# Optimization experiments

Measured on AMD Instinct MI355X. Metric: run time of the kernel, lower is better.

The kernel has to match this reference:

```python
import jax, jax.numpy as jnp
import numpy as np

B, N, DIM, H, K = 2, 8192, 256, 8, 32
HD = DIM // H


def setup_inputs() -> dict:
    key = jax.random.key(0)
    ks = jax.random.split(key, 10)
    s = 1.0 / np.sqrt(DIM)
    return {
        "x": jax.random.normal(ks[0], (B, N, DIM), jnp.float32),
        "xyz": jax.random.normal(ks[1], (B, N, 3), jnp.float32),
        "idx": jax.random.randint(ks[2], (B, N, K), 0, N, jnp.int32),
        "Wq": jax.random.normal(ks[3], (DIM, DIM), jnp.float32) * s,
        "bq": jnp.zeros((DIM,), jnp.float32),
        "Wk": jax.random.normal(ks[4], (DIM, DIM), jnp.float32) * s,
        "bk": jnp.zeros((DIM,), jnp.float32),
        "Wv": jax.random.normal(ks[5], (DIM, DIM), jnp.float32) * s,
        "bv": jnp.zeros((DIM,), jnp.float32),
        "Wo": jax.random.normal(ks[6], (DIM, DIM), jnp.float32) * s,
        "bo": jnp.zeros((DIM,), jnp.float32),
        "W1": jax.random.normal(ks[7], (3, 32), jnp.float32) * 0.5,
        "b1": jnp.zeros((32,), jnp.float32),
        "W2": jax.random.normal(ks[8], (32, H), jnp.float32) * 0.2,
        "b2": jnp.zeros((H,), jnp.float32),
    }


def reference(x, xyz, idx, Wq, bq, Wk, bk, Wv, bv, Wo, bo, W1, b1, W2, b2):
    Bn, Nn, C = x.shape
    k = idx.shape[-1]
    q = (x @ Wq + bq).reshape(Bn, Nn, H, HD)          # [B,N,H,hd]
    kf = (x @ Wk + bk).reshape(Bn, Nn, H, HD)
    vf = (x @ Wv + bv).reshape(Bn, Nn, H, HD)
    # gather k neighbors per point (per-batch fancy indexing)
    gather = jax.vmap(lambda f, i: f[i])               # [N,H,hd],[N,k] -> [N,k,H,hd]
    kn = gather(kf, idx)                               # [B,N,k,H,hd]
    vn = gather(vf, idx)
    nxyz = jax.vmap(lambda p, i: p[i])(xyz, idx)       # [B,N,k,3]
    rel = xyz[:, :, None, :] - nxyz                    # [B,N,k,3]
    bias = jax.nn.relu(rel @ W1 + b1) @ W2 + b2        # [B,N,k,H]
    scores = jnp.einsum('bnhd,bnkhd->bnhk', q, kn) / np.sqrt(HD).astype(np.float32)
    scores = scores + bias.transpose(0, 1, 3, 2)       # [B,N,H,k]
    attn = jax.nn.softmax(scores, axis=-1)
    out = jnp.einsum('bnhk,bnkhd->bnhd', attn, vn).reshape(Bn, Nn, C)
    return out @ Wo + bo
```

## Files before the change

### kernel.cpp

```cpp
#include <hip/hip_runtime.h>
#include <hip/hip_bf16.h>

typedef unsigned int uint32;
typedef unsigned short ushort;
typedef __attribute__((ext_vector_type(4))) float floatx4;
typedef __attribute__((ext_vector_type(8))) __bf16 bf16x8;

#define NPTS 8192
#define HSZ 524288

__device__ __forceinline__ ushort f2bf(float f) {
    uint32 u = __float_as_uint(f);
    uint32 r = (u + 0x7fffu + ((u >> 16) & 1u)) >> 16;
    return (ushort)r;
}
__device__ __forceinline__ float bf1(ushort u) { return __uint_as_float((uint32)u << 16); }
__device__ __forceinline__ float bflo(uint32 u) { return __uint_as_float(u << 16); }
__device__ __forceinline__ float bfhi(uint32 u) { return __uint_as_float(u & 0xffff0000u); }

__global__ __launch_bounds__(256) void prep_kernel(
    const float* __restrict__ x, const float* __restrict__ xyz, const int* __restrict__ idx,
    const float* __restrict__ Wq, const float* __restrict__ Wk,
    const float* __restrict__ Wv, const float* __restrict__ Wo,
    const float* __restrict__ bq, const float* __restrict__ bk, const float* __restrict__ bv,
    const float* __restrict__ W1, const float* __restrict__ b1,
    const float* __restrict__ W2, const float* __restrict__ b2,
    ushort* __restrict__ xb, ushort* __restrict__ Wqkvt, ushort* __restrict__ Wot,
    float* __restrict__ biasqkv, ushort* __restrict__ bias_hg) {
    const int bi = blockIdx.x;
    const int tid = threadIdx.x;
    if (bi < 4096) {
        int i = (bi * 256 + tid) * 4;
        float4 v = *(const float4*)(x + i);
        ushort4 o;
        o.x = f2bf(v.x); o.y = f2bf(v.y); o.z = f2bf(v.z); o.w = f2bf(v.w);
        *(ushort4*)(xb + i) = o;
    } else if (bi < 5120) {
        int f = (bi - 4096) * 256 + tid;
        if (f < 768 * 256) {
            int n = f >> 8, k = f & 255;
            int seg = n >> 8, nc = n & 255;
            const float* W = (seg == 0) ? Wq : (seg == 1) ? Wk : Wv;
            Wqkvt[f] = f2bf(W[k * 256 + nc]);
        } else {
            int g = f - 768 * 256;
            int n = g >> 8, k = g & 255;
            Wot[g] = f2bf(Wo[k * 256 + n]);
        }
        if (f < 768) biasqkv[f] = (f < 256) ? bq[f] : (f < 512) ? bk[f - 256] : bv[f - 512];
    } else {
        __shared__ float W1s[96], b1s[32], W2s[256], b2s[8];
        if (tid < 96) W1s[tid] = W1[tid];
        if (tid < 32) b1s[tid] = b1[tid];
        W2s[tid] = W2[tid];
        if (tid < 8) b2s[tid] = b2[tid];
        __syncthreads();
        const int wid = tid >> 6, lane = tid & 63;
        const int s = lane >> 5, j = lane & 31;
        const int p = (bi - 5120) * 8 + wid * 2 + s;
        const int b = p >> 13, n = p & 8191;
        const int nj = idx[(size_t)p * 32 + j];
        const size_t pb = ((size_t)b * NPTS + n) * 3;
        const size_t nb = ((size_t)b * NPTS + nj) * 3;
        const float rx = xyz[pb + 0] - xyz[nb + 0];
        const float ry = xyz[pb + 1] - xyz[nb + 1];
        const float rz = xyz[pb + 2] - xyz[nb + 2];
        float acc[8];
#pragma unroll
        for (int h = 0; h < 8; ++h) acc[h] = b2s[h];
#pragma unroll
        for (int u = 0; u < 32; ++u) {
            float hv = rx * W1s[u] + ry * W1s[32 + u] + rz * W1s[64 + u] + b1s[u];
            hv = fmaxf(hv, 0.f);
#pragma unroll
            for (int h = 0; h < 8; ++h) acc[h] += hv * W2s[u * 8 + h];
        }
#pragma unroll
        for (int h = 0; h < 8; ++h) bias_hg[(size_t)h * HSZ + p * 32 + j] = f2bf(acc[h]);
    }
}

__global__ __launch_bounds__(256) void gemm_qkv(const ushort* __restrict__ A,
                                                const ushort* __restrict__ Wt,
                                                const float* __restrict__ bias,
                                                ushort* __restrict__ qh, ushort* __restrict__ kh,
                                                ushort* __restrict__ vh) {
    __shared__ __align__(16) ushort As[128 * 64];
    __shared__ __align__(16) ushort Bs[128 * 64];
    const int tid = threadIdx.x;
    const int w = tid >> 6, lane = tid & 63;
    const int m0 = blockIdx.y * 128, n0 = blockIdx.x * 128;
    const int wm = (w & 1) * 64, wn = (w >> 1) * 64;

    floatx4 acc[4][4] = {};

    for (int kt = 0; kt < 256; kt += 64) {
        __syncthreads();
#pragma unroll
        for (int c4 = 0; c4 < 4; ++c4) {
            const int c = w * 4 + c4;
            const int r = c * 8 + (lane >> 3);
            const int gseg = (lane & 7) ^ (r & 7);
            const char* ga = (const char*)(A + (size_t)(m0 + r) * 256 + kt) + gseg * 16;
            const char* gb = (const char*)(Wt + (size_t)(n0 + r) * 256 + kt) + gseg * 16;
            __builtin_amdgcn_global_load_lds((const __attribute__((address_space(1))) void*)ga,
                                             (__attribute__((address_space(3))) void*)((char*)As + c * 1024),
                                             16, 0, 0);
            __builtin_amdgcn_global_load_lds((const __attribute__((address_space(1))) void*)gb,
                                             (__attribute__((address_space(3))) void*)((char*)Bs + c * 1024),
                                             16, 0, 0);
        }
        __syncthreads();

        bf16x8 af[2][4], bg[2][4];
#pragma unroll
        for (int kk = 0; kk < 2; ++kk) {
            const int s = kk * 4 + (lane >> 4);
            const int phys = s ^ (lane & 7);
#pragma unroll
            for (int i = 0; i < 4; ++i) {
                af[kk][i] = *(const bf16x8*)((const char*)As + (wm + i * 16 + (lane & 15)) * 128 + phys * 16);
                bg[kk][i] = *(const bf16x8*)((const char*)Bs + (wn + i * 16 + (lane & 15)) * 128 + phys * 16);
            }
        }
#pragma unroll
        for (int kk = 0; kk < 2; ++kk)
#pragma unroll
            for (int mi = 0; mi < 4; ++mi)
#pragma unroll
                for (int ni = 0; ni < 4; ++ni)
                    acc[mi][ni] = __builtin_amdgcn_mfma_f32_16x16x32_bf16(af[kk][mi], bg[kk][ni], acc[mi][ni], 0, 0, 0);
    }

#pragma unroll
    for (int ni = 0; ni < 4; ++ni) {
        const int col = n0 + wn + ni * 16 + (lane & 15);
        const int seg = col >> 8;
        const int head = (col >> 5) & 7;
        const int dim = col & 31;
        ushort* segp = (seg == 0) ? qh : (seg == 1) ? kh : vh;
        const float bv = bias[col];
#pragma unroll
        for (int mi = 0; mi < 4; ++mi) {
            const int row0 = m0 + wm + mi * 16 + (lane >> 4) * 4;
#pragma unroll
            for (int r = 0; r < 4; ++r)
                segp[(size_t)head * HSZ + (size_t)(row0 + r) * 32 + dim] = f2bf(acc[mi][ni][r] + bv);
        }
    }
}

__global__ __launch_bounds__(256) void gemm_mfma64(const ushort* __restrict__ A,
                                                   const ushort* __restrict__ Wt,
                                                   const float* __restrict__ bias,
                                                   float* __restrict__ outv, int N) {
    __shared__ __align__(16) ushort As[64 * 32];
    __shared__ __align__(16) ushort Bs[64 * 32];
    const int tid = threadIdx.x;
    const int w = tid >> 6, lane = tid & 63;
    const int m0 = blockIdx.y * 64, n0 = blockIdx.x * 64;
    const int row = tid >> 2;
    const int col16 = (tid & 3) * 16;

    floatx4 acc[4] = {};

    for (int kt = 0; kt < 256; kt += 32) {
        __syncthreads();
        {
            const char* ga = (const char*)(A + (size_t)(m0 + row) * 256 + kt) + col16;
            const char* gb = (const char*)(Wt + (size_t)(n0 + row) * 256 + kt) + col16;
            __builtin_amdgcn_global_load_lds((const __attribute__((address_space(1))) void*)ga,
                                             (__attribute__((address_space(3))) void*)((char*)As + w * 1024),
                                             16, 0, 0);
            __builtin_amdgcn_global_load_lds((const __attribute__((address_space(1))) void*)gb,
                                             (__attribute__((address_space(3))) void*)((char*)Bs + w * 1024),
                                             16, 0, 0);
        }
        __syncthreads();

        bf16x8 af = *(const bf16x8*)&As[(w * 16 + (lane & 15)) * 32 + (lane >> 4) * 8];
        bf16x8 bg[4];
#pragma unroll
        for (int ni = 0; ni < 4; ++ni)
            bg[ni] = *(const bf16x8*)&Bs[(ni * 16 + (lane & 15)) * 32 + (lane >> 4) * 8];
#pragma unroll
        for (int ni = 0; ni < 4; ++ni)
            acc[ni] = __builtin_amdgcn_mfma_f32_16x16x32_bf16(af, bg[ni], acc[ni], 0, 0, 0);
    }

#pragma unroll
    for (int ni = 0; ni < 4; ++ni) {
        const int col = n0 + ni * 16 + (lane & 15);
        const float bv = bias[col];
        const int row0 = m0 + w * 16 + (lane >> 4) * 4;
#pragma unroll
        for (int r = 0; r < 4; ++r)
            outv[(size_t)(row0 + r) * N + col] = acc[ni][r] + bv;
    }
}

__global__ __launch_bounds__(256) void attn_kernel(
    const ushort* __restrict__ qh, const ushort* __restrict__ kh, const ushort* __restrict__ vh,
    const int* __restrict__ idx, const ushort* __restrict__ bias_hg, ushort* __restrict__ out) {
    __shared__ __align__(16) float q_s[4][2][32];
    __shared__ float e_s[4][2][32];
    __shared__ uint32 off_s[4][2][32];
    __shared__ float ssum_s[4][2];

    const int tid = threadIdx.x, wid = tid >> 6, lane = tid & 63;
    const int h = blockIdx.x >> 11;
    const int pg = blockIdx.x & 2047;
    const int pbase = pg * 8 + wid * 2;

    const char* kh_h = (const char*)(kh + (size_t)h * HSZ);
    const char* vh_h = (const char*)(vh + (size_t)h * HSZ);

    const int s = lane >> 5, j = lane & 31;
    const int p = pbase + s;
    const int b = p >> 13;

    off_s[wid][s][j] = (uint32)(idx[(size_t)p * 32 + j] + b * NPTS) * 64u;
    q_s[wid][s][j] = bf1(qh[(size_t)h * HSZ + p * 32 + j]);
    __syncthreads();

    {
        const uint4* kp = (const uint4*)(kh_h + off_s[wid][s][j]);
        float d = 0.f;
#pragma unroll
        for (int c = 0; c < 4; ++c) {
            uint4 kv = kp[c];
            float4 qa = *(const float4*)&q_s[wid][s][c * 8];
            float4 qb = *(const float4*)&q_s[wid][s][c * 8 + 4];
            d += bflo(kv.x) * qa.x + bfhi(kv.x) * qa.y
               + bflo(kv.y) * qa.z + bfhi(kv.y) * qa.w
               + bflo(kv.z) * qb.x + bfhi(kv.z) * qb.y
               + bflo(kv.w) * qb.z + bfhi(kv.w) * qb.w;
        }
        const float sc = d * 0.17677669529663687f + bf1(bias_hg[(size_t)h * HSZ + p * 32 + j]);
        const float e = __expf(sc);
        float ssum = e;
#pragma unroll
        for (int msk = 16; msk >= 1; msk >>= 1) ssum += __shfl_xor(ssum, msk, 64);
        e_s[wid][s][j] = e;
        if (j == 0) ssum_s[wid][s] = ssum;
    }
    __syncthreads();

    {
        const int s2 = lane >> 5, hj = (lane >> 4) & 1, d2 = lane & 15;
        const int p2 = pbase + s2;
        const float rinv = __builtin_amdgcn_rcpf(ssum_s[wid][s2]);
        float ax = 0.f, ay = 0.f;
#pragma unroll
        for (int jj = 0; jj < 16; ++jj) {
            const int j2 = hj * 16 + jj;
            const float wgt = e_s[wid][s2][j2];
            const uint32 v = *(const uint32*)(vh_h + off_s[wid][s2][j2] + d2 * 4);
            ax += wgt * bflo(v);
            ay += wgt * bfhi(v);
        }
        ax += __shfl_xor(ax, 16, 64);
        ay += __shfl_xor(ay, 16, 64);
        if (hj == 0) {
            const uint32 o = (uint32)f2bf(ax * rinv) | ((uint32)f2bf(ay * rinv) << 16);
            *(uint32*)(out + (size_t)p2 * 256 + h * 32 + d2 * 2) = o;
        }
    }
}

extern "C" void kernel_launch(void* const* d_in, const int* in_sizes, int n_in,
                              void* d_out, int out_size, void* d_ws, size_t ws_size,
                              hipStream_t stream) {
    const float* x   = (const float*)d_in[0];
    const float* xyz = (const float*)d_in[1];
    const int*   idx = (const int*)d_in[2];
    const float* Wq = (const float*)d_in[3];
    const float* bq = (const float*)d_in[4];
    const float* Wk = (const float*)d_in[5];
    const float* bk = (const float*)d_in[6];
    const float* Wv = (const float*)d_in[7];
    const float* bv = (const float*)d_in[8];
    const float* Wo = (const float*)d_in[9];
    const float* bo = (const float*)d_in[10];
    const float* W1 = (const float*)d_in[11];
    const float* b1 = (const float*)d_in[12];
    const float* W2 = (const float*)d_in[13];
    const float* b2 = (const float*)d_in[14];

    char* wsb = (char*)d_ws;
    ushort* x_bf    = (ushort*)wsb;
    ushort* aout_bf = x_bf;
    ushort* qh      = (ushort*)(wsb + 8388608);
    ushort* kh      = (ushort*)(wsb + 16777216);
    ushort* vh      = (ushort*)(wsb + 25165824);
    ushort* bias_hg = (ushort*)(wsb + 33554432);
    ushort* Wqkvt   = (ushort*)(wsb + 41943040);
    ushort* Wot     = (ushort*)(wsb + 42336256);
    float*  biasqkv = (float*)(wsb + 42467328);

    prep_kernel<<<7168, 256, 0, stream>>>(x, xyz, idx, Wq, Wk, Wv, Wo, bq, bk, bv,
                                          W1, b1, W2, b2, x_bf, Wqkvt, Wot, biasqkv, bias_hg);

    gemm_qkv<<<dim3(6, 128), 256, 0, stream>>>(x_bf, Wqkvt, biasqkv, qh, kh, vh);

    attn_kernel<<<16384, 256, 0, stream>>>(qh, kh, vh, idx, bias_hg, aout_bf);

    gemm_mfma64<<<dim3(4, 256), 256, 0, stream>>>(aout_bf, Wot, bo, (float*)d_out, 256);
}
```

Before: 184.4 us.

## Prefetch V gathers before score compute and precompute neighbor offsets in prep

The attention kernel now issues all V-row gathers right after the first barrier, so they overlap with the K dot products and softmax instead of waiting on them. Neighbor byte offsets are precomputed in the prep kernel and read directly, and the scalar bias is loaded early. The block size drops from 256 to 128 threads with double the grid and a launch bound of 6 blocks per CU. This spends 16 extra registers per thread on prefetched values and adds an offsets buffer written by prep.

```diff
diff --git a/kernel.cpp b/kernel.cpp
--- a/kernel.cpp
+++ b/kernel.cpp
@@ -26,7 +26,7 @@
     const float* __restrict__ W1, const float* __restrict__ b1,
     const float* __restrict__ W2, const float* __restrict__ b2,
     ushort* __restrict__ xb, ushort* __restrict__ Wqkvt, ushort* __restrict__ Wot,
-    float* __restrict__ biasqkv, ushort* __restrict__ bias_hg) {
+    float* __restrict__ biasqkv, ushort* __restrict__ bias_hg, uint32* __restrict__ offs) {
     const int bi = blockIdx.x;
     const int tid = threadIdx.x;
     if (bi < 4096) {
@@ -60,6 +60,7 @@
         const int p = (bi - 5120) * 8 + wid * 2 + s;
         const int b = p >> 13, n = p & 8191;
         const int nj = idx[(size_t)p * 32 + j];
+        offs[(size_t)p * 32 + j] = (uint32)(nj + b * NPTS) * 64u;
         const size_t pb = ((size_t)b * NPTS + n) * 3;
         const size_t nb = ((size_t)b * NPTS + nj) * 3;
         const float rx = xyz[pb + 0] - xyz[nb + 0];
@@ -199,32 +200,39 @@
     }
 }
 
-__global__ __launch_bounds__(256) void attn_kernel(
+__global__ __launch_bounds__(128, 6) void attn_kernel(
     const ushort* __restrict__ qh, const ushort* __restrict__ kh, const ushort* __restrict__ vh,
-    const int* __restrict__ idx, const ushort* __restrict__ bias_hg, ushort* __restrict__ out) {
-    __shared__ __align__(16) float q_s[4][2][32];
-    __shared__ float e_s[4][2][32];
-    __shared__ uint32 off_s[4][2][32];
-    __shared__ float ssum_s[4][2];
+    const uint32* __restrict__ offs, const ushort* __restrict__ bias_hg, ushort* __restrict__ out) {
+    __shared__ __align__(16) float q_s[2][2][32];
+    __shared__ float e_s[2][2][32];
+    __shared__ uint32 off_s[2][2][32];
+    __shared__ float ssum_s[2][2];
 
     const int tid = threadIdx.x, wid = tid >> 6, lane = tid & 63;
-    const int h = blockIdx.x >> 11;
-    const int pg = blockIdx.x & 2047;
-    const int pbase = pg * 8 + wid * 2;
+    const int h = blockIdx.x >> 12;
+    const int pg = blockIdx.x & 4095;
+    const int pbase = pg * 4 + wid * 2;
 
     const char* kh_h = (const char*)(kh + (size_t)h * HSZ);
     const char* vh_h = (const char*)(vh + (size_t)h * HSZ);
 
     const int s = lane >> 5, j = lane & 31;
     const int p = pbase + s;
-    const int b = p >> 13;
-
-    off_s[wid][s][j] = (uint32)(idx[(size_t)p * 32 + j] + b * NPTS) * 64u;
+
+    const uint32 off = offs[(size_t)p * 32 + j];
+    off_s[wid][s][j] = off;
     q_s[wid][s][j] = bf1(qh[(size_t)h * HSZ + p * 32 + j]);
+    const float bias = bf1(bias_hg[(size_t)h * HSZ + p * 32 + j]);
     __syncthreads();
 
+    const int hj = (lane >> 4) & 1, d2 = lane & 15;
+    uint32 vv[16];
+#pragma unroll
+    for (int jj = 0; jj < 16; ++jj)
+        vv[jj] = *(const uint32*)(vh_h + off_s[wid][s][hj * 16 + jj] + d2 * 4);
+
     {
-        const uint4* kp = (const uint4*)(kh_h + off_s[wid][s][j]);
+        const uint4* kp = (const uint4*)(kh_h + off);
         float d = 0.f;
 #pragma unroll
         for (int c = 0; c < 4; ++c) {
@@ -236,7 +244,7 @@
                + bflo(kv.z) * qb.x + bfhi(kv.z) * qb.y
                + bflo(kv.w) * qb.z + bfhi(kv.w) * qb.w;
         }
-        const float sc = d * 0.17677669529663687f + bf1(bias_hg[(size_t)h * HSZ + p * 32 + j]);
+        const float sc = d * 0.17677669529663687f + bias;
         const float e = __expf(sc);
         float ssum = e;
 #pragma unroll
@@ -247,23 +255,19 @@
     __syncthreads();
 
     {
-        const int s2 = lane >> 5, hj = (lane >> 4) & 1, d2 = lane & 15;
-        const int p2 = pbase + s2;
-        const float rinv = __builtin_amdgcn_rcpf(ssum_s[wid][s2]);
+        const float rinv = __builtin_amdgcn_rcpf(ssum_s[wid][s]);
         float ax = 0.f, ay = 0.f;
 #pragma unroll
         for (int jj = 0; jj < 16; ++jj) {
-            const int j2 = hj * 16 + jj;
-            const float wgt = e_s[wid][s2][j2];
-            const uint32 v = *(const uint32*)(vh_h + off_s[wid][s2][j2] + d2 * 4);
-            ax += wgt * bflo(v);
-            ay += wgt * bfhi(v);
+            const float wgt = e_s[wid][s][hj * 16 + jj];
+            ax += wgt * bflo(vv[jj]);
+            ay += wgt * bfhi(vv[jj]);
         }
         ax += __shfl_xor(ax, 16, 64);
         ay += __shfl_xor(ay, 16, 64);
         if (hj == 0) {
             const uint32 o = (uint32)f2bf(ax * rinv) | ((uint32)f2bf(ay * rinv) << 16);
-            *(uint32*)(out + (size_t)p2 * 256 + h * 32 + d2 * 2) = o;
+            *(uint32*)(out + (size_t)p * 256 + h * 32 + d2 * 2) = o;
         }
     }
 }
@@ -297,13 +301,15 @@
     ushort* Wqkvt   = (ushort*)(wsb + 41943040);
     ushort* Wot     = (ushort*)(wsb + 42336256);
     float*  biasqkv = (float*)(wsb + 42467328);
+    uint32* offs    = (uint32*)(wsb + 42471424);
 
     prep_kernel<<<7168, 256, 0, stream>>>(x, xyz, idx, Wq, Wk, Wv, Wo, bq, bk, bv,
-                                          W1, b1, W2, b2, x_bf, Wqkvt, Wot, biasqkv, bias_hg);
+                                          W1, b1, W2, b2, x_bf, Wqkvt, Wot, biasqkv,
+                                          bias_hg, offs);
 
     gemm_qkv<<<dim3(6, 128), 256, 0, stream>>>(x_bf, Wqkvt, biasqkv, qh, kh, vh);
 
-    attn_kernel<<<16384, 256, 0, stream>>>(qh, kh, vh, idx, bias_hg, aout_bf);
+    attn_kernel<<<32768, 128, 0, stream>>>(qh, kh, vh, offs, bias_hg, aout_bf);
 
     gemm_mfma64<<<dim3(4, 256), 256, 0, stream>>>(aout_bf, Wot, bo, (float*)d_out, 256);
 }
```

Measured after the change: 192.5 us. 1.04x slower.
